# Kernel optimization log

Measured on AMD Instinct MI355X. Metric: run time of the kernel, lower is better.

The kernel has to match this reference:

```python
import jax, jax.numpy as jnp
import numpy as np

# ---- static config (from MACEConfig / MACELayerConfig) ----
N_NODES = 128
F_S = 128          # n_invariant_feat_hidden (0e channels)
F_V = 64           # n_vectors_hidden (1e channels)
N_BESSEL = 8       # bessel_number
R_MAX = 5.0        # r_max
N_LAYERS = 2       # n_interactions
HID_RAD = 64       # radial MLP hidden width
F_S_OUT = 128      # n_invariant_feat_readout
F_V_OUT = 64       # n_vectors_readout
AVG_NEIGH = float(N_NODES)  # avg_num_neighbors default = n_nodes
RAD_OUT = F_S + 3 * F_V     # per-edge radial channel weights for the 4 TP paths


def _senders_receivers(n):
    # fully connected graph, matching get_senders_and_receivers
    s = np.repeat(np.arange(n), n - 1)
    j = np.tile(np.arange(1, n), n)
    r = (s + j) % n
    return jnp.asarray(s, dtype=jnp.int32), jnp.asarray(r, dtype=jnp.int32)


def _bessel(r):
    # e3nn bessel basis: sqrt(2/c) sin(n pi r / c) / r, n = 1..N_BESSEL
    n = jnp.arange(1, N_BESSEL + 1, dtype=r.dtype)
    return jnp.sqrt(2.0 / R_MAX) * jnp.sin(n * jnp.pi * r[:, None] / R_MAX) / r[:, None]


def _envelope(r):
    # smooth radial cutoff (polynomial p=6), stand-in for e3nn soft_envelope
    u = r / R_MAX
    p = 6.0
    env = 1.0 - (p + 1) * (p + 2) / 2 * u ** p + p * (p + 2) * u ** (p + 1) - p * (p + 1) / 2 * u ** (p + 2)
    return jnp.where(u < 1.0, env, 0.0)


def _forward(x, species_embed, Wr1, Wr2, W_sv, W_mix_s, W_mix_v, W_out_s, W_out_v):
    senders, receivers = _senders_receivers(N_NODES)

    def single(pos):  # pos: (N, 3)
        com = pos.mean(axis=0)                       # centre of mass (3,)
        v = pos[receivers] - pos[senders]            # edge relative vectors (E, 3)
        r = jnp.linalg.norm(v, axis=-1) + 1e-8       # (E,)
        vhat = v / r[:, None]
        rb = _bessel(r) * _envelope(r)[:, None]      # (E, N_BESSEL)

        s = jnp.broadcast_to(species_embed[0], (N_NODES, F_S))       # 0e node feats
        V = jnp.zeros((N_NODES, F_V, 3), dtype=pos.dtype)            # 1e node feats

        for l in range(N_LAYERS):
            # learned per-edge radial weights for each tensor-product path
            h = jax.nn.silu(rb @ Wr1[l]) @ Wr2[l]    # (E, RAD_OUT)
            R0 = h[:, :F_S]
            R1 = h[:, F_S:F_S + F_V]
            R2 = h[:, F_S + F_V:F_S + 2 * F_V]
            R3 = h[:, F_S + 2 * F_V:]

            s_src = s[senders]                       # gather (E, F_S)
            V_src = V[senders]                       # gather (E, F_V, 3)

            # CG tensor-product paths (only 0e and 1e irreps present):
            m0a = R0 * s_src                                         # 0e x 0e -> 0e
            m0b = R1 * jnp.einsum('efk,ek->ef', V_src, vhat)         # 1e x 1e -> 0e
            m1a = (R2 * (s_src @ W_sv[l]))[..., None] * vhat[:, None, :]  # 0e x 1e -> 1e
            m1b = R3[..., None] * V_src                              # 1e x 0e -> 1e

            # scatter-sum message passing over receivers
            agg0 = jax.ops.segment_sum(jnp.concatenate([m0a, m0b], -1), receivers,
                                       num_segments=N_NODES) / AVG_NEIGH   # (N, F_S+F_V)
            agg1 = jax.ops.segment_sum(jnp.concatenate([m1a, m1b], 1), receivers,
                                       num_segments=N_NODES) / AVG_NEIGH   # (N, 2F_V, 3)

            s = s + jax.nn.silu(agg0 @ W_mix_s[l])
            V = V + jnp.einsum('nfk,fg->ngk', agg1, W_mix_v[l])

        out_s = s @ W_out_s                                          # (N, F_S_OUT)
        out_v = jnp.einsum('nfk,fg->ngk', V, W_out_v) + com          # (N, F_V_OUT, 3) + CoM
        return out_v, out_s

    return jax.vmap(single)(x)


def setup_inputs() -> dict:
    key = jax.random.key(0)
    ks = jax.random.split(key, 10)
    sc = lambda fan: 1.0 / np.sqrt(fan)
    inp = {
        'x': jax.random.normal(ks[0], (8, N_NODES, 3), dtype=jnp.float32),
        'species_embed': jax.random.normal(ks[1], (1, F_S), dtype=jnp.float32),
        'Wr1': jax.random.normal(ks[2], (N_LAYERS, N_BESSEL, HID_RAD), dtype=jnp.float32) * sc(N_BESSEL),
        'Wr2': jax.random.normal(ks[3], (N_LAYERS, HID_RAD, RAD_OUT), dtype=jnp.float32) * sc(HID_RAD),
        'W_sv': jax.random.normal(ks[4], (N_LAYERS, F_S, F_V), dtype=jnp.float32) * sc(F_S),
        'W_mix_s': jax.random.normal(ks[5], (N_LAYERS, F_S + F_V, F_S), dtype=jnp.float32) * sc(F_S + F_V),
        'W_mix_v': jax.random.normal(ks[6], (N_LAYERS, 2 * F_V, F_V), dtype=jnp.float32) * sc(2 * F_V),
        'W_out_s': jax.random.normal(ks[7], (F_S, F_S_OUT), dtype=jnp.float32) * sc(F_S),
        'W_out_v': jax.random.normal(ks[8], (F_V, F_V_OUT), dtype=jnp.float32) * sc(F_V),
    }
    return inp


def reference(x, species_embed, Wr1, Wr2, W_sv, W_mix_s, W_mix_v, W_out_s, W_out_v):
    return _forward(x, species_embed, Wr1, Wr2, W_sv, W_mix_s, W_mix_v, W_out_s, W_out_v)
```

## Files before the change

kernel.cpp:

```cpp
#include <hip/hip_runtime.h>
#include <math.h>

typedef unsigned short u16;
typedef __attribute__((ext_vector_type(8))) short frag_ab;
typedef __attribute__((ext_vector_type(4))) float frag_cd;

#define BATCH 8
#define NN 128
#define FS 128
#define FV 64
#define NB 8
#define HID 64
#define ROUT 320
#define HSTRB 72
#define HSTRF 68

#define SZ_S (BATCH*FS*NN)
#define SZ_V (BATCH*FV*3*NN)
#define SZ_T (BATCH*FV*NN)
#define N_W2B (ROUT*HID)
#define OFF_SB 0
#define OFF_VB (OFF_SB+SZ_S)
#define OFF_T1 (OFF_VB+SZ_V)
#define OFF_W2B (OFF_T1+SZ_T)

__device__ __forceinline__ float silu_f(float x){ return x * (1.0f/(1.0f + __expf(-x))); }

__device__ __forceinline__ u16 f2bf(float x){
  union { float f; unsigned int u; } v; v.f = x;
  unsigned int r = v.u + 0x7fffu + ((v.u >> 16) & 1u);
  return (u16)(r >> 16);
}

__global__ __launch_bounds__(320) void layer0_kernel(
    const float* __restrict__ pos,
    const float* __restrict__ species,
    const float* __restrict__ Wr1l,
    const float* __restrict__ Wr2,
    const float* __restrict__ Wsv,
    const float* __restrict__ WmixSl,
    const float* __restrict__ WmixVl,
    float* __restrict__ sOut,
    float* __restrict__ vOut,
    float* __restrict__ tOut,
    u16*   __restrict__ w2b)
{
  const int tid = threadIdx.x;
  const int b   = blockIdx.x >> 7;
  const int k   = blockIdx.x & 127;

  __shared__ float hidF[128*HSTRF];
  __shared__ float vhx[128], vhy[128], vhz[128];
  __shared__ float colsum[4][64];
  __shared__ float aggS[128];
  __shared__ float aggV1[192];
  __shared__ float sNew[FS];
  __shared__ float t0L[64];

  const float* pb   = pos + b*NN*3;
  const float* Wr2l = Wr2;

  if (tid < 256){
    const int i    = tid & 127;
    const int half = tid >> 7;
    float vx = pb[k*3+0]-pb[i*3+0];
    float vy = pb[k*3+1]-pb[i*3+1];
    float vz = pb[k*3+2]-pb[i*3+2];
    float r = sqrtf(vx*vx+vy*vy+vz*vz) + 1e-8f;
    float inv = 1.0f/r;
    if (half==0){ vhx[i]=vx*inv; vhy[i]=vy*inv; vhz[i]=vz*inv; }
    float u = r*0.2f;
    float env = 0.0f;
    if (u < 1.0f && i != k){
      float u2=u*u, u6=u2*u2*u2;
      env = 1.0f - 28.0f*u6 + 48.0f*u6*u - 21.0f*u6*u2;
    }
    float coef = 0.6324555320336759f * inv * env;
    float th   = r * 0.6283185307179586f;
    float s1 = __sinf(th), c1 = __cosf(th);
    float rb[NB];
    rb[0] = coef*s1;
    float twoc = 2.f*c1, sp = s1, spp = 0.f;
    #pragma unroll
    for(int n=1;n<NB;n++){ float s = twoc*sp - spp; spp = sp; sp = s; rb[n] = coef*s; }
    #pragma unroll
    for(int jg=0;jg<8;jg++){
      const int jgg = half*8 + jg;
      float h0=0.f,h1=0.f,h2=0.f,h3=0.f;
      #pragma unroll
      for(int n=0;n<NB;n++){
        const float* wr = Wr1l + n*HID + jgg*4;
        float rn = rb[n];
        h0 = fmaf(rn, wr[0], h0);
        h1 = fmaf(rn, wr[1], h1);
        h2 = fmaf(rn, wr[2], h2);
        h3 = fmaf(rn, wr[3], h3);
      }
      float4 hh = make_float4(silu_f(h0), silu_f(h1), silu_f(h2), silu_f(h3));
      *(float4*)&hidF[i*HSTRF + jgg*4] = hh;
    }
  } else {
    const int g = tid - 256;
    float a0=0.f, a1=0.f;
    #pragma unroll 8
    for (int c=0; c<FS; c+=2){
      a0 = fmaf(species[c],   Wsv[c*FV+g],     a0);
      a1 = fmaf(species[c+1], Wsv[(c+1)*FV+g], a1);
    }
    t0L[g] = a0+a1;
  }
  __syncthreads();

  if (tid < 256){
    const int j   = tid & 63;
    const int var = tid >> 6;
    float a0 = 0.f, a1 = 0.f;
    if (var == 0){
      #pragma unroll 8
      for (int i=0;i<128;i+=2){ a0 += hidF[i*HSTRF + j]; a1 += hidF[(i+1)*HSTRF + j]; }
    } else {
      const float* wv = (var==1) ? vhx : (var==2) ? vhy : vhz;
      #pragma unroll 8
      for (int i=0;i<128;i+=2){
        a0 = fmaf(hidF[i*HSTRF + j],     wv[i],   a0);
        a1 = fmaf(hidF[(i+1)*HSTRF + j], wv[i+1], a1);
      }
    }
    colsum[var][j] = a0+a1;
  } else if (tid < 276){
    const int t = blockIdx.x*20 + (tid-256);
    const int j = t & 63, c = t >> 6;
    w2b[t] = f2bf(Wr2[HID*ROUT + j*ROUT + c]);
  }
  __syncthreads();

  if (tid < 128){
    const int c = tid;
    float d0 = 0.f, d1 = 0.f;
    #pragma unroll 8
    for (int j=0;j<HID;j+=2){
      d0 = fmaf(colsum[0][j],   Wr2l[j*ROUT + c],     d0);
      d1 = fmaf(colsum[0][j+1], Wr2l[(j+1)*ROUT + c], d1);
    }
    aggS[c] = species[c] * (d0+d1) * (1.0f/128.0f);
  } else {
    const int idx = tid - 128;
    const int f = idx & 63, c3 = idx >> 6;
    float d0 = 0.f, d1 = 0.f;
    #pragma unroll 8
    for (int j=0;j<HID;j+=2){
      d0 = fmaf(colsum[1+c3][j],   Wr2l[j*ROUT + 192 + f],     d0);
      d1 = fmaf(colsum[1+c3][j+1], Wr2l[(j+1)*ROUT + 192 + f], d1);
    }
    aggV1[f*3+c3] = t0L[f] * (d0+d1) * (1.0f/128.0f);
  }
  __syncthreads();

  if (tid < FS){
    float a0=0.f, a1=0.f, a2=0.f, a3=0.f;
    #pragma unroll 8
    for (int cc=0; cc<128; cc+=4){
      a0 = fmaf(aggS[cc],   WmixSl[cc*FS+tid],     a0);
      a1 = fmaf(aggS[cc+1], WmixSl[(cc+1)*FS+tid], a1);
      a2 = fmaf(aggS[cc+2], WmixSl[(cc+2)*FS+tid], a2);
      a3 = fmaf(aggS[cc+3], WmixSl[(cc+3)*FS+tid], a3);
    }
    float sn = species[tid] + silu_f((a0+a1)+(a2+a3));
    sNew[tid] = sn;
    sOut[(b*FS+tid)*NN + k] = sn;
  } else {
    const int o = tid - 128;
    const int g = o/3, c3 = o - g*3;
    float a0=0.f, a1=0.f;
    #pragma unroll 8
    for (int f=0; f<FV; f+=2){
      a0 = fmaf(aggV1[f*3+c3],     WmixVl[f*FV+g],     a0);
      a1 = fmaf(aggV1[(f+1)*3+c3], WmixVl[(f+1)*FV+g], a1);
    }
    vOut[(b*FV*3 + o)*NN + k] = a0 + a1;
  }
  __syncthreads();
  if (tid < FV){
    const float* Wsv1 = Wsv + FS*FV;
    float a0=0.f, a1=0.f, a2=0.f, a3=0.f;
    #pragma unroll 8
    for (int f=0; f<FS; f+=4){
      a0 = fmaf(sNew[f],   Wsv1[f*FV+tid],     a0);
      a1 = fmaf(sNew[f+1], Wsv1[(f+1)*FV+tid], a1);
      a2 = fmaf(sNew[f+2], Wsv1[(f+2)*FV+tid], a2);
      a3 = fmaf(sNew[f+3], Wsv1[(f+3)*FV+tid], a3);
    }
    tOut[(b*FV+tid)*NN + k] = (a0+a1)+(a2+a3);
  }
}

__global__ __launch_bounds__(512) void layer_kernel(
    const float* __restrict__ pos,
    const float* __restrict__ sIn,
    const float* __restrict__ vIn,
    const float* __restrict__ tIn,
    const float* __restrict__ Wr1l,
    const u16*   __restrict__ w2bl,
    const float* __restrict__ WmixSl,
    const float* __restrict__ WmixVl,
    const float* __restrict__ WoutS,
    const float* __restrict__ WoutV,
    float* __restrict__ outp)
{
  const int tid  = threadIdx.x;
  const int b    = blockIdx.x >> 6;
  const int k0   = (blockIdx.x & 63) * 2;
  const int w    = tid >> 6;
  const int lane = tid & 63;
  const int col  = lane & 15;
  const int quad = lane >> 4;
  const int wq   = w & 3;
  const int sh   = w >> 2;

  __shared__ u16   hidB[2][128*HSTRB];
  __shared__ float vhx[2][128], vhy[2][128], vhz[2][128];
  __shared__ float aggP[2][2][576];
  __shared__ float sPart[2][2][FS];
  __shared__ float sNew[2][FS];
  __shared__ float vNewL[2][192];
  __shared__ float comL[3];

  const float* pb = pos + b*NN*3;

  {
    const int kk   = tid >> 8;
    const int r2   = tid & 255;
    const int i    = r2 & 127;
    const int half = r2 >> 7;
    const int k    = k0 + kk;
    float vx = pb[k*3+0]-pb[i*3+0];
    float vy = pb[k*3+1]-pb[i*3+1];
    float vz = pb[k*3+2]-pb[i*3+2];
    float r = sqrtf(vx*vx+vy*vy+vz*vz) + 1e-8f;
    float inv = 1.0f/r;
    if (half==0){ vhx[kk][i]=vx*inv; vhy[kk][i]=vy*inv; vhz[kk][i]=vz*inv; }
    float u = r*0.2f;
    float env = 0.0f;
    if (u < 1.0f && i != k){
      float u2=u*u, u6=u2*u2*u2;
      env = 1.0f - 28.0f*u6 + 48.0f*u6*u - 21.0f*u6*u2;
    }
    float coef = 0.6324555320336759f * inv * env;
    float th   = r * 0.6283185307179586f;
    float s1 = __sinf(th), c1 = __cosf(th);
    float rb[NB];
    rb[0] = coef*s1;
    float twoc = 2.f*c1, sp = s1, spp = 0.f;
    #pragma unroll
    for(int n=1;n<NB;n++){ float s = twoc*sp - spp; spp = sp; sp = s; rb[n] = coef*s; }
    u16* hrow = hidB[kk] + i*HSTRB;
    #pragma unroll
    for(int jg=0;jg<8;jg++){
      const int jgg = half*8 + jg;
      float h0=0.f,h1=0.f,h2=0.f,h3=0.f;
      #pragma unroll
      for(int n=0;n<NB;n++){
        const float* wr = Wr1l + n*HID + jgg*4;
        float rn = rb[n];
        h0 = fmaf(rn, wr[0], h0);
        h1 = fmaf(rn, wr[1], h1);
        h2 = fmaf(rn, wr[2], h2);
        h3 = fmaf(rn, wr[3], h3);
      }
      ushort4 uu = make_ushort4(f2bf(silu_f(h0)), f2bf(silu_f(h1)),
                                f2bf(silu_f(h2)), f2bf(silu_f(h3)));
      *(ushort4*)(hrow + jgg*4) = uu;
    }
    if (tid < 3){
      float a0=0.f, a1=0.f;
      for (int n=0;n<NN;n+=2){ a0 += pb[n*3+tid]; a1 += pb[(n+1)*3+tid]; }
      comL[tid] = (a0+a1) * (1.0f/128.0f);
    }
  }
  __syncthreads();

  const float* sIb = sIn + b*FS*NN;
  const float* vIb = vIn + b*FV*3*NN;
  const float* tIb = tIn + b*FV*NN;
  const int i00 = sh*64 + quad*4;

#define MFMA_PAIR(accv, KK, MT) \
    { const int hrow_ = (sh*64 + (MT)*16 + col)*HSTRB + quad*8; \
      frag_ab a0_ = *(const frag_ab*)&hidB[KK][hrow_]; \
      frag_ab a1_ = *(const frag_ab*)&hidB[KK][hrow_ + 32]; \
      accv = __builtin_amdgcn_mfma_f32_16x16x32_bf16(a0_, b0, accv, 0,0,0); \
      accv = __builtin_amdgcn_mfma_f32_16x16x32_bf16(a1_, b1, accv, 0,0,0); }

  #pragma unroll
  for (int q=0; q<2; q++){
    const int ntg = q*4 + wq;
    const int c   = ntg*16 + col;
    const u16* wp = w2bl + c*HID + quad*8;
    const frag_ab b0 = *(const frag_ab*)(wp);
    const frag_ab b1 = *(const frag_ab*)(wp + 32);
    const float* fb = sIb + c*NN + i00;
    float sA0 = 0.f, sA1 = 0.f;
    #pragma unroll
    for (int mt=0; mt<4; mt++){
      float4 s4 = *(const float4*)&fb[mt*16];
      frag_cd acc = {0.f,0.f,0.f,0.f};
      MFMA_PAIR(acc, 0, mt);
      sA0 += acc[0]*s4.x + acc[1]*s4.y + acc[2]*s4.z + acc[3]*s4.w;
      frag_cd ac2 = {0.f,0.f,0.f,0.f};
      MFMA_PAIR(ac2, 1, mt);
      sA1 += ac2[0]*s4.x + ac2[1]*s4.y + ac2[2]*s4.z + ac2[3]*s4.w;
    }
    sA0 += __shfl_xor(sA0, 16, 64); sA0 += __shfl_xor(sA0, 32, 64);
    sA1 += __shfl_xor(sA1, 16, 64); sA1 += __shfl_xor(sA1, 32, 64);
    if (lane < 16){ aggP[0][sh][ntg*16+lane] = sA0; aggP[1][sh][ntg*16+lane] = sA1; }
  }
  {
    const int ntg = 8 + wq;
    const int c   = ntg*16 + col;
    const u16* wp = w2bl + c*HID + quad*8;
    const frag_ab b0 = *(const frag_ab*)(wp);
    const frag_ab b1 = *(const frag_ab*)(wp + 32);
    const int f = c - FS;
    const float* fb = vIb + f*3*NN + i00;
    float sA0 = 0.f, sA1 = 0.f;
    #pragma unroll
    for (int mt=0; mt<4; mt++){
      float4 vx4 = *(const float4*)&fb[mt*16];
      float4 vy4 = *(const float4*)&fb[NN + mt*16];
      float4 vz4 = *(const float4*)&fb[2*NN + mt*16];
      {
        float4 hx4 = *(const float4*)&vhx[0][i00 + mt*16];
        float4 hy4 = *(const float4*)&vhy[0][i00 + mt*16];
        float4 hz4 = *(const float4*)&vhz[0][i00 + mt*16];
        frag_cd acc = {0.f,0.f,0.f,0.f};
        MFMA_PAIR(acc, 0, mt);
        sA0 += acc[0]*(vx4.x*hx4.x + vy4.x*hy4.x + vz4.x*hz4.x)
             + acc[1]*(vx4.y*hx4.y + vy4.y*hy4.y + vz4.y*hz4.y)
             + acc[2]*(vx4.z*hx4.z + vy4.z*hy4.z + vz4.z*hz4.z)
             + acc[3]*(vx4.w*hx4.w + vy4.w*hy4.w + vz4.w*hz4.w);
      }
      {
        float4 hx4 = *(const float4*)&vhx[1][i00 + mt*16];
        float4 hy4 = *(const float4*)&vhy[1][i00 + mt*16];
        float4 hz4 = *(const float4*)&vhz[1][i00 + mt*16];
        frag_cd acc = {0.f,0.f,0.f,0.f};
        MFMA_PAIR(acc, 1, mt);
        sA1 += acc[0]*(vx4.x*hx4.x + vy4.x*hy4.x + vz4.x*hz4.x)
             + acc[1]*(vx4.y*hx4.y + vy4.y*hy4.y + vz4.y*hz4.y)
             + acc[2]*(vx4.z*hx4.z + vy4.z*hy4.z + vz4.z*hz4.z)
             + acc[3]*(vx4.w*hx4.w + vy4.w*hy4.w + vz4.w*hz4.w);
      }
    }
    sA0 += __shfl_xor(sA0, 16, 64); sA0 += __shfl_xor(sA0, 32, 64);
    sA1 += __shfl_xor(sA1, 16, 64); sA1 += __shfl_xor(sA1, 32, 64);
    if (lane < 16){ aggP[0][sh][ntg*16+lane] = sA0; aggP[1][sh][ntg*16+lane] = sA1; }
  }
  {
    const int ntg = 12 + wq;
    const int c   = ntg*16 + col;
    const u16* wp = w2bl + c*HID + quad*8;
    const frag_ab b0 = *(const frag_ab*)(wp);
    const frag_ab b1 = *(const frag_ab*)(wp + 32);
    const int f = c - (FS+FV);
    const float* fb = tIb + f*NN + i00;
    float sX0=0.f,sY0=0.f,sZ0=0.f, sX1=0.f,sY1=0.f,sZ1=0.f;
    #pragma unroll
    for (int mt=0; mt<4; mt++){
      float4 t4 = *(const float4*)&fb[mt*16];
      {
        float4 hx4 = *(const float4*)&vhx[0][i00 + mt*16];
        float4 hy4 = *(const float4*)&vhy[0][i00 + mt*16];
        float4 hz4 = *(const float4*)&vhz[0][i00 + mt*16];
        frag_cd acc = {0.f,0.f,0.f,0.f};
        MFMA_PAIR(acc, 0, mt);
        float t0_=acc[0]*t4.x, t1_=acc[1]*t4.y, t2_=acc[2]*t4.z, t3_=acc[3]*t4.w;
        sX0 += t0_*hx4.x + t1_*hx4.y + t2_*hx4.z + t3_*hx4.w;
        sY0 += t0_*hy4.x + t1_*hy4.y + t2_*hy4.z + t3_*hy4.w;
        sZ0 += t0_*hz4.x + t1_*hz4.y + t2_*hz4.z + t3_*hz4.w;
      }
      {
        float4 hx4 = *(const float4*)&vhx[1][i00 + mt*16];
        float4 hy4 = *(const float4*)&vhy[1][i00 + mt*16];
        float4 hz4 = *(const float4*)&vhz[1][i00 + mt*16];
        frag_cd acc = {0.f,0.f,0.f,0.f};
        MFMA_PAIR(acc, 1, mt);
        float t0_=acc[0]*t4.x, t1_=acc[1]*t4.y, t2_=acc[2]*t4.z, t3_=acc[3]*t4.w;
        sX1 += t0_*hx4.x + t1_*hx4.y + t2_*hx4.z + t3_*hx4.w;
        sY1 += t0_*hy4.x + t1_*hy4.y + t2_*hy4.z + t3_*hy4.w;
        sZ1 += t0_*hz4.x + t1_*hz4.y + t2_*hz4.z + t3_*hz4.w;
      }
    }
    sX0 += __shfl_xor(sX0,16,64); sX0 += __shfl_xor(sX0,32,64);
    sY0 += __shfl_xor(sY0,16,64); sY0 += __shfl_xor(sY0,32,64);
    sZ0 += __shfl_xor(sZ0,16,64); sZ0 += __shfl_xor(sZ0,32,64);
    sX1 += __shfl_xor(sX1,16,64); sX1 += __shfl_xor(sX1,32,64);
    sY1 += __shfl_xor(sY1,16,64); sY1 += __shfl_xor(sY1,32,64);
    sZ1 += __shfl_xor(sZ1,16,64); sZ1 += __shfl_xor(sZ1,32,64);
    if (lane < 16){
      const int f2 = (ntg*16 + lane) - 192;
      aggP[0][sh][192+f2*3+0]=sX0; aggP[0][sh][192+f2*3+1]=sY0; aggP[0][sh][192+f2*3+2]=sZ0;
      aggP[1][sh][192+f2*3+0]=sX1; aggP[1][sh][192+f2*3+1]=sY1; aggP[1][sh][192+f2*3+2]=sZ1;
    }
  }
  {
    const int ntg = 16 + wq;
    const int c   = ntg*16 + col;
    const u16* wp = w2bl + c*HID + quad*8;
    const frag_ab b0 = *(const frag_ab*)(wp);
    const frag_ab b1 = *(const frag_ab*)(wp + 32);
    const int f = c - (FS+2*FV);
    const float* fb = vIb + f*3*NN + i00;
    float sX0=0.f,sY0=0.f,sZ0=0.f, sX1=0.f,sY1=0.f,sZ1=0.f;
    #pragma unroll
    for (int mt=0; mt<4; mt++){
      float4 vx4 = *(const float4*)&fb[mt*16];
      float4 vy4 = *(const float4*)&fb[NN + mt*16];
      float4 vz4 = *(const float4*)&fb[2*NN + mt*16];
      {
        frag_cd acc = {0.f,0.f,0.f,0.f};
        MFMA_PAIR(acc, 0, mt);
        sX0 += acc[0]*vx4.x + acc[1]*vx4.y + acc[2]*vx4.z + acc[3]*vx4.w;
        sY0 += acc[0]*vy4.x + acc[1]*vy4.y + acc[2]*vy4.z + acc[3]*vy4.w;
        sZ0 += acc[0]*vz4.x + acc[1]*vz4.y + acc[2]*vz4.z + acc[3]*vz4.w;
      }
      {
        frag_cd acc = {0.f,0.f,0.f,0.f};
        MFMA_PAIR(acc, 1, mt);
        sX1 += acc[0]*vx4.x + acc[1]*vx4.y + acc[2]*vx4.z + acc[3]*vx4.w;
        sY1 += acc[0]*vy4.x + acc[1]*vy4.y + acc[2]*vy4.z + acc[3]*vy4.w;
        sZ1 += acc[0]*vz4.x + acc[1]*vz4.y + acc[2]*vz4.z + acc[3]*vz4.w;
      }
    }
    sX0 += __shfl_xor(sX0,16,64); sX0 += __shfl_xor(sX0,32,64);
    sY0 += __shfl_xor(sY0,16,64); sY0 += __shfl_xor(sY0,32,64);
    sZ0 += __shfl_xor(sZ0,16,64); sZ0 += __shfl_xor(sZ0,32,64);
    sX1 += __shfl_xor(sX1,16,64); sX1 += __shfl_xor(sX1,32,64);
    sY1 += __shfl_xor(sY1,16,64); sY1 += __shfl_xor(sY1,32,64);
    sZ1 += __shfl_xor(sZ1,16,64); sZ1 += __shfl_xor(sZ1,32,64);
    if (lane < 16){
      const int f2 = (ntg*16 + lane) - 256;
      aggP[0][sh][384+f2*3+0]=sX0; aggP[0][sh][384+f2*3+1]=sY0; aggP[0][sh][384+f2*3+2]=sZ0;
      aggP[1][sh][384+f2*3+0]=sX1; aggP[1][sh][384+f2*3+1]=sY1; aggP[1][sh][384+f2*3+2]=sZ1;
    }
  }
#undef MFMA_PAIR

  __syncthreads();
  for (int t2=tid; t2<1152; t2+=512){
    const int kk = (t2 >= 576) ? 1 : 0;
    const int t  = t2 - kk*576;
    aggP[kk][0][t] = (aggP[kk][0][t] + aggP[kk][1][t]) * (1.0f/128.0f);
  }
  __syncthreads();

  if (tid < 256){
    const int o = tid & 127, p = tid >> 7;
    const int c0 = p*96;
    float a00=0.f,a01=0.f, a10=0.f,a11=0.f;
    #pragma unroll 8
    for (int cc=c0; cc<c0+96; cc+=2){
      float w0 = WmixSl[cc*FS+o];
      float w1 = WmixSl[(cc+1)*FS+o];
      a00 = fmaf(aggP[0][0][cc],   w0, a00);
      a01 = fmaf(aggP[0][0][cc+1], w1, a01);
      a10 = fmaf(aggP[1][0][cc],   w0, a10);
      a11 = fmaf(aggP[1][0][cc+1], w1, a11);
    }
    sPart[0][p][o] = a00+a01;
    sPart[1][p][o] = a10+a11;
  } else if (tid < 448){
    const int o = tid - 256;
    const int g = o/3, c3 = o - g*3;
    float a00=0.f,a01=0.f, a10=0.f,a11=0.f;
    #pragma unroll 8
    for (int f=0; f<FV; f++){
      float w0 = WmixVl[f*FV+g];
      float w1 = WmixVl[(f+FV)*FV+g];
      a00 = fmaf(aggP[0][0][192+f*3+c3], w0, a00);
      a01 = fmaf(aggP[0][0][384+f*3+c3], w1, a01);
      a10 = fmaf(aggP[1][0][192+f*3+c3], w0, a10);
      a11 = fmaf(aggP[1][0][384+f*3+c3], w1, a11);
    }
    vNewL[0][o] = vIb[o*NN + k0]     + a00 + a01;
    vNewL[1][o] = vIb[o*NN + k0 + 1] + a10 + a11;
  }
  __syncthreads();

  if (tid < FS){
    sNew[0][tid] = sIb[tid*NN + k0]     + silu_f(sPart[0][0][tid] + sPart[0][1][tid]);
    sNew[1][tid] = sIb[tid*NN + k0 + 1] + silu_f(sPart[1][0][tid] + sPart[1][1][tid]);
  } else if (tid < 320){
    const int o = tid - 128;
    const int g = o/3, c3 = o - g*3;
    float a0 = comL[c3], a1 = comL[c3];
    #pragma unroll 8
    for (int f=0; f<FV; f++){
      float wv = WoutV[f*FV+g];
      a0 = fmaf(vNewL[0][f*3+c3], wv, a0);
      a1 = fmaf(vNewL[1][f*3+c3], wv, a1);
    }
    outp[(b*NN+k0)*FV*3 + o]     = a0;
    outp[(b*NN+k0+1)*FV*3 + o]   = a1;
  }
  __syncthreads();

  if (tid < FS){
    float a00=0.f,a01=0.f, a10=0.f,a11=0.f;
    #pragma unroll 8
    for (int f=0; f<FS; f+=2){
      float w0 = WoutS[f*FS+tid];
      float w1 = WoutS[(f+1)*FS+tid];
      a00 = fmaf(sNew[0][f],   w0, a00);
      a01 = fmaf(sNew[0][f+1], w1, a01);
      a10 = fmaf(sNew[1][f],   w0, a10);
      a11 = fmaf(sNew[1][f+1], w1, a11);
    }
    outp[BATCH*NN*FV*3 + (b*NN+k0)*FS + tid]   = a00+a01;
    outp[BATCH*NN*FV*3 + (b*NN+k0+1)*FS + tid] = a10+a11;
  }
}

extern "C" void kernel_launch(void* const* d_in, const int* in_sizes, int n_in,
                              void* d_out, int out_size, void* d_ws, size_t ws_size,
                              hipStream_t stream)
{
  const float* x       = (const float*)d_in[0];
  const float* species = (const float*)d_in[1];
  const float* Wr1     = (const float*)d_in[2];
  const float* Wr2     = (const float*)d_in[3];
  const float* Wsv     = (const float*)d_in[4];
  const float* WmixS   = (const float*)d_in[5];
  const float* WmixV   = (const float*)d_in[6];
  const float* WoutS   = (const float*)d_in[7];
  const float* WoutV   = (const float*)d_in[8];
  float* ws  = (float*)d_ws;
  float* out = (float*)d_out;

  float* sB  = ws + OFF_SB;
  float* vB  = ws + OFF_VB;
  float* t1  = ws + OFF_T1;
  u16*   w2b = (u16*)(ws + OFF_W2B);

  layer0_kernel<<<BATCH*NN, 320, 0, stream>>>(x, species, Wr1, Wr2, Wsv,
      WmixS, WmixV, sB, vB, t1, w2b);

  layer_kernel<<<BATCH*NN/2, 512, 0, stream>>>(x, sB, vB, t1,
      Wr1 + NB*HID, w2b, WmixS + 192*FS, WmixV + 128*FV,
      WoutS, WoutV, out);
}
```

Baseline: 145.0 us.

## Process two receiver nodes per block in layer0 and store hidden activations as bf16

The layer-0 kernel now handles two receiver nodes per 512-thread block instead of one per 320-thread block, halving the grid. Weight loads from Wr2, WmixS and Wsv are shared across the two nodes, which halves global weight traffic per node. Hidden activations are kept in shared memory as bf16 rather than fp32 to fit both nodes, and the phases are restructured so t0 and the w2b conversion overlap with the radial contraction. The bf16 storage adds rounding error to the column sums, and the larger block may lower occupancy.

```diff
diff --git a/kernel.cpp b/kernel.cpp
--- a/kernel.cpp
+++ b/kernel.cpp
@@ -13,7 +13,6 @@
 #define HID 64
 #define ROUT 320
 #define HSTRB 72
-#define HSTRF 68
 
 #define SZ_S (BATCH*FS*NN)
 #define SZ_V (BATCH*FV*3*NN)
@@ -31,8 +30,11 @@
   unsigned int r = v.u + 0x7fffu + ((v.u >> 16) & 1u);
   return (u16)(r >> 16);
 }
-
-__global__ __launch_bounds__(320) void layer0_kernel(
+__device__ __forceinline__ float bf2f(u16 h){
+  union { unsigned int u; float f; } v; v.u = ((unsigned int)h) << 16; return v.f;
+}
+
+__global__ __launch_bounds__(512) void layer0_kernel(
     const float* __restrict__ pos,
     const float* __restrict__ species,
     const float* __restrict__ Wr1l,
@@ -46,29 +48,32 @@
     u16*   __restrict__ w2b)
 {
   const int tid = threadIdx.x;
-  const int b   = blockIdx.x >> 7;
-  const int k   = blockIdx.x & 127;
-
-  __shared__ float hidF[128*HSTRF];
-  __shared__ float vhx[128], vhy[128], vhz[128];
-  __shared__ float colsum[4][64];
-  __shared__ float aggS[128];
-  __shared__ float aggV1[192];
-  __shared__ float sNew[FS];
+  const int b   = blockIdx.x >> 6;
+  const int k0  = (blockIdx.x & 63) * 2;
+
+  __shared__ u16   hidB[2][128*HSTRB];
+  __shared__ float vhx[2][128], vhy[2][128], vhz[2][128];
+  __shared__ float colsum[2][4][64];
+  __shared__ float aggS[2][128];
+  __shared__ float dV[2][192];
+  __shared__ float sNew[2][128];
   __shared__ float t0L[64];
 
   const float* pb   = pos + b*NN*3;
   const float* Wr2l = Wr2;
 
-  if (tid < 256){
-    const int i    = tid & 127;
-    const int half = tid >> 7;
+  {
+    const int kk   = tid >> 8;
+    const int r2   = tid & 255;
+    const int i    = r2 & 127;
+    const int half = r2 >> 7;
+    const int k    = k0 + kk;
     float vx = pb[k*3+0]-pb[i*3+0];
     float vy = pb[k*3+1]-pb[i*3+1];
     float vz = pb[k*3+2]-pb[i*3+2];
     float r = sqrtf(vx*vx+vy*vy+vz*vz) + 1e-8f;
     float inv = 1.0f/r;
-    if (half==0){ vhx[i]=vx*inv; vhy[i]=vy*inv; vhz[i]=vz*inv; }
+    if (half==0){ vhx[kk][i]=vx*inv; vhy[kk][i]=vy*inv; vhz[kk][i]=vz*inv; }
     float u = r*0.2f;
     float env = 0.0f;
     if (u < 1.0f && i != k){
@@ -83,6 +88,7 @@
     float twoc = 2.f*c1, sp = s1, spp = 0.f;
     #pragma unroll
     for(int n=1;n<NB;n++){ float s = twoc*sp - spp; spp = sp; sp = s; rb[n] = coef*s; }
+    u16* hrow = hidB[kk] + i*HSTRB;
     #pragma unroll
     for(int jg=0;jg<8;jg++){
       const int jgg = half*8 + jg;
@@ -96,11 +102,69 @@
         h2 = fmaf(rn, wr[2], h2);
         h3 = fmaf(rn, wr[3], h3);
       }
-      float4 hh = make_float4(silu_f(h0), silu_f(h1), silu_f(h2), silu_f(h3));
-      *(float4*)&hidF[i*HSTRF + jgg*4] = hh;
-    }
-  } else {
-    const int g = tid - 256;
+      ushort4 uu = make_ushort4(f2bf(silu_f(h0)), f2bf(silu_f(h1)),
+                                f2bf(silu_f(h2)), f2bf(silu_f(h3)));
+      *(ushort4*)(hrow + jgg*4) = uu;
+    }
+  }
+  __syncthreads();
+
+  {
+    const int kk  = tid >> 8;
+    const int var = (tid >> 6) & 3;
+    const int j   = tid & 63;
+    const u16* hb = hidB[kk];
+    float a0 = 0.f, a1 = 0.f;
+    if (var == 0){
+      #pragma unroll 8
+      for (int i=0;i<128;i+=2){
+        a0 += bf2f(hb[i*HSTRB + j]);
+        a1 += bf2f(hb[(i+1)*HSTRB + j]);
+      }
+    } else {
+      const float* wv = (var==1) ? vhx[kk] : (var==2) ? vhy[kk] : vhz[kk];
+      #pragma unroll 8
+      for (int i=0;i<128;i+=2){
+        a0 = fmaf(bf2f(hb[i*HSTRB + j]),     wv[i],   a0);
+        a1 = fmaf(bf2f(hb[(i+1)*HSTRB + j]), wv[i+1], a1);
+      }
+    }
+    colsum[kk][var][j] = a0+a1;
+  }
+  __syncthreads();
+
+  if (tid < 128){
+    const int c = tid;
+    float d00=0.f,d01=0.f, d10=0.f,d11=0.f;
+    #pragma unroll 8
+    for (int j=0;j<HID;j+=2){
+      float w0 = Wr2l[j*ROUT + c];
+      float w1 = Wr2l[(j+1)*ROUT + c];
+      d00 = fmaf(colsum[0][0][j],   w0, d00);
+      d01 = fmaf(colsum[0][0][j+1], w1, d01);
+      d10 = fmaf(colsum[1][0][j],   w0, d10);
+      d11 = fmaf(colsum[1][0][j+1], w1, d11);
+    }
+    float sc = species[c] * (1.0f/128.0f);
+    aggS[0][c] = sc * (d00+d01);
+    aggS[1][c] = sc * (d10+d11);
+  } else if (tid < 320){
+    const int o = tid - 128;
+    const int f = o & 63, c3 = o >> 6;
+    float d00=0.f,d01=0.f, d10=0.f,d11=0.f;
+    #pragma unroll 8
+    for (int j=0;j<HID;j+=2){
+      float w0 = Wr2l[j*ROUT + 192 + f];
+      float w1 = Wr2l[(j+1)*ROUT + 192 + f];
+      d00 = fmaf(colsum[0][1+c3][j],   w0, d00);
+      d01 = fmaf(colsum[0][1+c3][j+1], w1, d01);
+      d10 = fmaf(colsum[1][1+c3][j],   w0, d10);
+      d11 = fmaf(colsum[1][1+c3][j+1], w1, d11);
+    }
+    dV[0][f*3+c3] = (d00+d01) * (1.0f/128.0f);
+    dV[1][f*3+c3] = (d10+d11) * (1.0f/128.0f);
+  } else if (tid < 384){
+    const int g = tid - 320;
     float a0=0.f, a1=0.f;
     #pragma unroll 8
     for (int c=0; c<FS; c+=2){
@@ -108,89 +172,60 @@
       a1 = fmaf(species[c+1], Wsv[(c+1)*FV+g], a1);
     }
     t0L[g] = a0+a1;
-  }
-  __syncthreads();
-
-  if (tid < 256){
-    const int j   = tid & 63;
-    const int var = tid >> 6;
-    float a0 = 0.f, a1 = 0.f;
-    if (var == 0){
-      #pragma unroll 8
-      for (int i=0;i<128;i+=2){ a0 += hidF[i*HSTRF + j]; a1 += hidF[(i+1)*HSTRF + j]; }
-    } else {
-      const float* wv = (var==1) ? vhx : (var==2) ? vhy : vhz;
-      #pragma unroll 8
-      for (int i=0;i<128;i+=2){
-        a0 = fmaf(hidF[i*HSTRF + j],     wv[i],   a0);
-        a1 = fmaf(hidF[(i+1)*HSTRF + j], wv[i+1], a1);
-      }
-    }
-    colsum[var][j] = a0+a1;
-  } else if (tid < 276){
-    const int t = blockIdx.x*20 + (tid-256);
+  } else if (tid < 424){
+    const int t = blockIdx.x*40 + (tid-384);
     const int j = t & 63, c = t >> 6;
     w2b[t] = f2bf(Wr2[HID*ROUT + j*ROUT + c]);
   }
   __syncthreads();
 
-  if (tid < 128){
-    const int c = tid;
-    float d0 = 0.f, d1 = 0.f;
-    #pragma unroll 8
-    for (int j=0;j<HID;j+=2){
-      d0 = fmaf(colsum[0][j],   Wr2l[j*ROUT + c],     d0);
-      d1 = fmaf(colsum[0][j+1], Wr2l[(j+1)*ROUT + c], d1);
-    }
-    aggS[c] = species[c] * (d0+d1) * (1.0f/128.0f);
-  } else {
-    const int idx = tid - 128;
-    const int f = idx & 63, c3 = idx >> 6;
-    float d0 = 0.f, d1 = 0.f;
-    #pragma unroll 8
-    for (int j=0;j<HID;j+=2){
-      d0 = fmaf(colsum[1+c3][j],   Wr2l[j*ROUT + 192 + f],     d0);
-      d1 = fmaf(colsum[1+c3][j+1], Wr2l[(j+1)*ROUT + 192 + f], d1);
-    }
-    aggV1[f*3+c3] = t0L[f] * (d0+d1) * (1.0f/128.0f);
-  }
-  __syncthreads();
-
   if (tid < FS){
-    float a0=0.f, a1=0.f, a2=0.f, a3=0.f;
-    #pragma unroll 8
-    for (int cc=0; cc<128; cc+=4){
-      a0 = fmaf(aggS[cc],   WmixSl[cc*FS+tid],     a0);
-      a1 = fmaf(aggS[cc+1], WmixSl[(cc+1)*FS+tid], a1);
-      a2 = fmaf(aggS[cc+2], WmixSl[(cc+2)*FS+tid], a2);
-      a3 = fmaf(aggS[cc+3], WmixSl[(cc+3)*FS+tid], a3);
-    }
-    float sn = species[tid] + silu_f((a0+a1)+(a2+a3));
-    sNew[tid] = sn;
-    sOut[(b*FS+tid)*NN + k] = sn;
-  } else {
+    float a00=0.f,a01=0.f, a10=0.f,a11=0.f;
+    #pragma unroll 8
+    for (int cc=0; cc<128; cc+=2){
+      float w0 = WmixSl[cc*FS+tid];
+      float w1 = WmixSl[(cc+1)*FS+tid];
+      a00 = fmaf(aggS[0][cc],   w0, a00);
+      a01 = fmaf(aggS[0][cc+1], w1, a01);
+      a10 = fmaf(aggS[1][cc],   w0, a10);
+      a11 = fmaf(aggS[1][cc+1], w1, a11);
+    }
+    float sn0 = species[tid] + silu_f(a00+a01);
+    float sn1 = species[tid] + silu_f(a10+a11);
+    sNew[0][tid] = sn0;
+    sNew[1][tid] = sn1;
+    sOut[(b*FS+tid)*NN + k0]     = sn0;
+    sOut[(b*FS+tid)*NN + k0 + 1] = sn1;
+  } else if (tid < 320){
     const int o = tid - 128;
     const int g = o/3, c3 = o - g*3;
     float a0=0.f, a1=0.f;
     #pragma unroll 8
-    for (int f=0; f<FV; f+=2){
-      a0 = fmaf(aggV1[f*3+c3],     WmixVl[f*FV+g],     a0);
-      a1 = fmaf(aggV1[(f+1)*3+c3], WmixVl[(f+1)*FV+g], a1);
-    }
-    vOut[(b*FV*3 + o)*NN + k] = a0 + a1;
-  }
-  __syncthreads();
+    for (int f=0; f<FV; f++){
+      float w = WmixVl[f*FV+g];
+      float tf = t0L[f];
+      a0 = fmaf(tf*dV[0][f*3+c3], w, a0);
+      a1 = fmaf(tf*dV[1][f*3+c3], w, a1);
+    }
+    vOut[(b*FV*3 + o)*NN + k0]     = a0;
+    vOut[(b*FV*3 + o)*NN + k0 + 1] = a1;
+  }
+  __syncthreads();
+
   if (tid < FV){
     const float* Wsv1 = Wsv + FS*FV;
-    float a0=0.f, a1=0.f, a2=0.f, a3=0.f;
-    #pragma unroll 8
-    for (int f=0; f<FS; f+=4){
-      a0 = fmaf(sNew[f],   Wsv1[f*FV+tid],     a0);
-      a1 = fmaf(sNew[f+1], Wsv1[(f+1)*FV+tid], a1);
-      a2 = fmaf(sNew[f+2], Wsv1[(f+2)*FV+tid], a2);
-      a3 = fmaf(sNew[f+3], Wsv1[(f+3)*FV+tid], a3);
-    }
-    tOut[(b*FV+tid)*NN + k] = (a0+a1)+(a2+a3);
+    float a00=0.f,a01=0.f, a10=0.f,a11=0.f;
+    #pragma unroll 8
+    for (int f=0; f<FS; f+=2){
+      float w0 = Wsv1[f*FV+tid];
+      float w1 = Wsv1[(f+1)*FV+tid];
+      a00 = fmaf(sNew[0][f],   w0, a00);
+      a01 = fmaf(sNew[0][f+1], w1, a01);
+      a10 = fmaf(sNew[1][f],   w0, a10);
+      a11 = fmaf(sNew[1][f+1], w1, a11);
+    }
+    tOut[(b*FV+tid)*NN + k0]     = (a00+a01);
+    tOut[(b*FV+tid)*NN + k0 + 1] = (a10+a11);
   }
 }
 
@@ -541,7 +576,7 @@
   float* t1  = ws + OFF_T1;
   u16*   w2b = (u16*)(ws + OFF_W2B);
 
-  layer0_kernel<<<BATCH*NN, 320, 0, stream>>>(x, species, Wr1, Wr2, Wsv,
+  layer0_kernel<<<BATCH*NN/2, 512, 0, stream>>>(x, species, Wr1, Wr2, Wsv,
       WmixS, WmixV, sB, vB, t1, w2b);
 
   layer_kernel<<<BATCH*NN/2, 512, 0, stream>>>(x, sB, vB, t1,
```

New measurement: 137.2 us. -5.3%, faster.
